# Kernel tuning notes

Measured on AMD Instinct MI355X. Metric: run time of the kernel, lower is better.

Reference implementation:

```python
import jax, jax.numpy as jnp
import numpy as np

N_EMBED = 512
HEAD_SIZE = 64

def setup_inputs() -> dict:
    key = jax.random.key(0)
    k1, k2, k3, k4 = jax.random.split(key, 4)
    B, T, C, H = 4, 4096, N_EMBED, HEAD_SIZE
    x = jax.random.normal(k1, (B, T, C), dtype=jnp.float32)
    # nn.Linear(C, H, bias=False): weight shape [H, C]; y = x @ W.T
    scale = 1.0 / np.sqrt(C)
    Wq = jax.random.uniform(k2, (H, C), dtype=jnp.float32, minval=-scale, maxval=scale)
    Wk = jax.random.uniform(k3, (H, C), dtype=jnp.float32, minval=-scale, maxval=scale)
    Wv = jax.random.uniform(k4, (H, C), dtype=jnp.float32, minval=-scale, maxval=scale)
    return {"x": x, "Wq": Wq, "Wk": Wk, "Wv": Wv}

def reference(x, Wq, Wk, Wv) -> jnp.ndarray:
    B, T, C = x.shape
    q = jnp.einsum('btc,hc->bth', x, Wq)   # [B,T,H]
    k = jnp.einsum('btc,hc->bth', x, Wk)
    v = jnp.einsum('btc,hc->bth', x, Wv)
    # NOTE: original scales by n_embed**-0.5 (C), not head_size**-0.5
    wei = jnp.einsum('bth,bsh->bts', q, k) * (C ** -0.5)  # [B,T,T]
    causal = jnp.tril(jnp.ones((T, T), dtype=bool))
    wei = jnp.where(causal, wei, -jnp.inf)
    wei = jax.nn.softmax(wei, axis=-1)
    out = jnp.einsum('bts,bsh->bth', wei, v)  # [B,T,H]
    return out
```

## Files before the change

kernel.cpp:

```cpp
#include <hip/hip_runtime.h>

typedef float f32x4 __attribute__((ext_vector_type(4)));
typedef __bf16 bf16x8 __attribute__((ext_vector_type(8)));
typedef __bf16 bf16x4 __attribute__((ext_vector_type(4)));
typedef short short4v __attribute__((ext_vector_type(4)));

#define MFMA32K(a, b, c) __builtin_amdgcn_mfma_f32_16x16x32_bf16((a), (b), (c), 0, 0, 0)
#define MFMA16K(a, b, c) __builtin_amdgcn_mfma_f32_16x16x16bf16_1k((a), (b), (c), 0, 0, 0)
#define CFENCE() asm volatile("" ::: "memory")
#define DSFENCE() asm volatile("s_waitcnt lgkmcnt(0)" ::: "memory")

constexpr int Tn = 4096, Cn = 512, Hn = 64;
constexpr float QSCALE = 1.4426950408889634f * 0.04419417382415922f;
constexpr float M0 = -30000.0f;

__global__ void wconv(const float* __restrict__ Wq, const float* __restrict__ Wk,
                      const float* __restrict__ Wv, __bf16* __restrict__ Wb) {
    int t = blockIdx.y;
    int i = blockIdx.x * 256 + threadIdx.x;
    const float* src = (t == 0) ? Wq : (t == 1) ? Wk : Wv;
    float scale = (t == 0) ? QSCALE : 1.0f;
    Wb[t * Hn * Cn + i] = (__bf16)(src[i] * scale);
}

__device__ inline bf16x8 cvt8(float4 u0, float4 u1) {
    bf16x8 r;
    r[0] = (__bf16)u0.x; r[1] = (__bf16)u0.y; r[2] = (__bf16)u0.z; r[3] = (__bf16)u0.w;
    r[4] = (__bf16)u1.x; r[5] = (__bf16)u1.y; r[6] = (__bf16)u1.z; r[7] = (__bf16)u1.w;
    return r;
}

__global__ __launch_bounds__(256) void proj(const float* __restrict__ x,
                                            const __bf16* __restrict__ Wb,
                                            __bf16* __restrict__ Qb,
                                            __bf16* __restrict__ Kb,
                                            __bf16* __restrict__ VF) {
    const int tid = threadIdx.x;
    const int lane = tid & 63, wid = tid >> 6;
    const int c = lane & 15, h = lane >> 4;
    const int row0 = blockIdx.x * 64 + wid * 16;

    __shared__ __bf16 Ws[2][192 * 36];
    __shared__ __bf16 tb[4][16][72];

    f32x4 acc[3][4] = {};
    const float* xr = x + (size_t)(row0 + c) * Cn;

#pragma unroll
    for (int i = 0; i < 3; ++i) {
        int g = tid + i * 256, r = g >> 2, gc = g & 3;
        *(bf16x8*)&Ws[0][r * 36 + gc * 8] = *(const bf16x8*)(Wb + (size_t)r * Cn + gc * 8);
    }
    float4 xc0 = *(const float4*)(xr + 8 * h);
    float4 xc1 = *(const float4*)(xr + 8 * h + 4);
    __syncthreads();

#pragma unroll 2
    for (int ks = 0; ks < 16; ++ks) {
        const int cur = ks & 1;
        bf16x8 wreg[3];
        float4 xn0, xn1;
        if (ks < 15) {
#pragma unroll
            for (int i = 0; i < 3; ++i) {
                int g = tid + i * 256, r = g >> 2, gc = g & 3;
                wreg[i] = *(const bf16x8*)(Wb + (size_t)r * Cn + (ks + 1) * 32 + gc * 8);
            }
            xn0 = *(const float4*)(xr + (ks + 1) * 32 + 8 * h);
            xn1 = *(const float4*)(xr + (ks + 1) * 32 + 8 * h + 4);
        }
        bf16x8 a0 = cvt8(xc0, xc1);
#pragma unroll
        for (int w = 0; w < 3; ++w)
#pragma unroll
            for (int nt = 0; nt < 4; ++nt) {
                bf16x8 bf = *(const bf16x8*)&Ws[cur][(w * 64 + nt * 16 + c) * 36 + 8 * h];
                acc[w][nt] = MFMA32K(a0, bf, acc[w][nt]);
            }
        if (ks < 15) {
#pragma unroll
            for (int i = 0; i < 3; ++i) {
                int g = tid + i * 256, r = g >> 2, gc = g & 3;
                *(bf16x8*)&Ws[cur ^ 1][r * 36 + gc * 8] = wreg[i];
            }
            xc0 = xn0; xc1 = xn1;
        }
        __syncthreads();
    }

#pragma unroll
    for (int w = 0; w < 2; ++w) {
        CFENCE();
#pragma unroll
        for (int nt = 0; nt < 4; ++nt)
#pragma unroll
            for (int r = 0; r < 4; ++r)
                tb[wid][h * 4 + r][nt * 16 + c] = (__bf16)acc[w][nt][r];
        DSFENCE();
        __bf16* dst = (w == 0) ? Qb : Kb;
#pragma unroll
        for (int ch = 0; ch < 2; ++ch) {
            int rr = ch * 8 + (lane >> 3);
            bf16x8 vv = *(const bf16x8*)(&tb[wid][rr][(lane & 7) * 8]);
            *(bf16x8*)(dst + (size_t)(row0 + rr) * Hn + (lane & 7) * 8) = vv;
        }
        CFENCE();
    }

    const int b = row0 >> 12;
    const int t0 = row0 & (Tn - 1);
    const int tile = t0 >> 4;
#pragma unroll
    for (int nt = 0; nt < 4; ++nt) {
        f32x4 a = acc[2][nt];
        bf16x4 v4;
        v4[0] = (__bf16)a.x; v4[1] = (__bf16)a.y;
        v4[2] = (__bf16)a.z; v4[3] = (__bf16)a.w;
        size_t off = ((size_t)((b * 256 + tile) * 4 + h) * 64 + (nt * 16 + c)) * 4;
        *(bf16x4*)(VF + off) = v4;
    }
}

__global__ __launch_bounds__(512) void attn(const __bf16* __restrict__ Qb,
                                            const __bf16* __restrict__ Kb,
                                            const __bf16* __restrict__ VF,
                                            float* __restrict__ out) {
    const int tid = threadIdx.x;
    const int lane = tid & 63, ks = tid >> 6;
    const int c = lane & 15, h = lane >> 4;
    const int b = blockIdx.x & 3;
    const int v = blockIdx.x >> 2;

    const __bf16* Kbase = Kb + (size_t)b * Tn * Hn;
    const __bf16* Vbase = VF + (size_t)b * 256 * 1024;

    __shared__ float Mo[4][64][36];
    __shared__ float Mml[4][64][4];

#pragma unroll 1
    for (int grp = 0; grp < 2; ++grp) {
        const int vg = grp ? (127 - v) : v;
        const int qbase = vg * 32;
        const int nkv = vg / 2 + 1;

        bf16x8 qf[2][2];
#pragma unroll
        for (int qs = 0; qs < 2; ++qs) {
            const __bf16* qp = Qb + (size_t)(b * Tn + qbase + qs * 16 + c) * Hn;
            qf[qs][0] = *(const bf16x8*)(qp + 8 * h);
            qf[qs][1] = *(const bf16x8*)(qp + 32 + 8 * h);
        }

        f32x4 o[2][4] = {};
        float m[2] = {M0, M0};
        float l[2] = {};

        bf16x8 kfc[4][2];
        {
            const int kt0 = (ks < nkv) ? ks : nkv - 1;
#pragma unroll
            for (int ct = 0; ct < 4; ++ct) {
                const __bf16* kp = Kbase + (size_t)(kt0 * 64 + ct * 16 + c) * Hn;
                kfc[ct][0] = *(const bf16x8*)(kp + 8 * h);
                kfc[ct][1] = *(const bf16x8*)(kp + 32 + 8 * h);
            }
        }

        for (int kt = ks; kt < nkv; kt += 8) {
            const int j0 = kt * 64;
            bf16x8 kfn[4][2];
            {
                const int ktn = (kt + 8 < nkv) ? kt + 8 : kt;
#pragma unroll
                for (int ct = 0; ct < 4; ++ct) {
                    const __bf16* kp = Kbase + (size_t)(ktn * 64 + ct * 16 + c) * Hn;
                    kfn[ct][0] = *(const bf16x8*)(kp + 8 * h);
                    kfn[ct][1] = *(const bf16x8*)(kp + 32 + 8 * h);
                }
            }
            short4v vf[4][4];
            const __bf16* vt = Vbase + ((size_t)(j0 >> 4) << 10) + (h << 8);
#pragma unroll
            for (int dt = 0; dt < 4; ++dt)
#pragma unroll
                for (int ct = 0; ct < 4; ++ct)
                    vf[dt][ct] = *(const short4v*)(vt + (ct << 10) + ((dt * 16 + c) << 2));

            const bool diag = (kt == nkv - 1);

#pragma unroll
            for (int qs = 0; qs < 2; ++qs) {
                f32x4 s[4];
#pragma unroll
                for (int ct = 0; ct < 4; ++ct) {
                    f32x4 z = {};
                    z = MFMA32K(kfc[ct][0], qf[qs][0], z);
                    z = MFMA32K(kfc[ct][1], qf[qs][1], z);
                    s[ct] = z;
                }
                if (diag) {
#pragma unroll
                    for (int ct = 0; ct < 4; ++ct)
#pragma unroll
                        for (int r = 0; r < 4; ++r)
                            if (j0 + ct * 16 + 4 * h + r > qbase + qs * 16 + c)
                                s[ct][r] = -1e30f;
                }
                float lm = fmaxf(fmaxf(fmaxf(s[0][0], s[0][1]), fmaxf(s[0][2], s[0][3])),
                                 fmaxf(fmaxf(s[1][0], s[1][1]), fmaxf(s[1][2], s[1][3])));
                lm = fmaxf(lm, fmaxf(fmaxf(fmaxf(s[2][0], s[2][1]), fmaxf(s[2][2], s[2][3])),
                                     fmaxf(fmaxf(s[3][0], s[3][1]), fmaxf(s[3][2], s[3][3]))));
                if (!__all(lm <= m[qs] + 8.0f)) {
                    float rm = fmaxf(lm, __shfl_xor(lm, 16));
                    rm = fmaxf(rm, __shfl_xor(rm, 32));
                    float mn = fmaxf(m[qs], rm);
                    float sc = __builtin_amdgcn_exp2f(m[qs] - mn);
                    m[qs] = mn;
                    l[qs] *= sc;
#pragma unroll
                    for (int dt = 0; dt < 4; ++dt) o[qs][dt] *= sc;
                }
                short4v pf[4];
                float lsum = 0.0f;
#pragma unroll
                for (int ct = 0; ct < 4; ++ct) {
                    bf16x4 pb;
#pragma unroll
                    for (int r = 0; r < 4; ++r) {
                        float p = __builtin_amdgcn_exp2f(s[ct][r] - m[qs]);
                        lsum += p;
                        pb[r] = (__bf16)p;
                    }
                    pf[ct] = __builtin_bit_cast(short4v, pb);
                }
                l[qs] += lsum;
#pragma unroll
                for (int dt = 0; dt < 4; ++dt)
#pragma unroll
                    for (int ct = 0; ct < 4; ++ct)
                        o[qs][dt] = MFMA16K(vf[dt][ct], pf[ct], o[qs][dt]);
            }
#pragma unroll
            for (int ct = 0; ct < 4; ++ct) {
                kfc[ct][0] = kfn[ct][0];
                kfc[ct][1] = kfn[ct][1];
            }
        }

#pragma unroll
        for (int qs = 0; qs < 2; ++qs) {
            l[qs] += __shfl_xor(l[qs], 16);
            l[qs] += __shfl_xor(l[qs], 32);
        }

#pragma unroll
        for (int step = 4; step >= 1; step >>= 1) {
            if (ks >= step && ks < 2 * step) {
                int slot = ks - step;
#pragma unroll
                for (int qs = 0; qs < 2; ++qs) {
                    Mml[slot][lane][qs] = m[qs];
                    Mml[slot][lane][2 + qs] = l[qs];
#pragma unroll
                    for (int dt = 0; dt < 4; ++dt)
                        *(f32x4*)&Mo[slot][lane][(qs * 4 + dt) * 4] = o[qs][dt];
                }
            }
            __syncthreads();
            if (ks < step) {
#pragma unroll
                for (int qs = 0; qs < 2; ++qs) {
                    float m2 = Mml[ks][lane][qs];
                    float l2 = Mml[ks][lane][2 + qs];
                    float M = fmaxf(m[qs], m2);
                    float e1 = __builtin_amdgcn_exp2f(m[qs] - M);
                    float e2 = __builtin_amdgcn_exp2f(m2 - M);
                    m[qs] = M;
                    l[qs] = l[qs] * e1 + l2 * e2;
#pragma unroll
                    for (int dt = 0; dt < 4; ++dt) {
                        f32x4 o2 = *(const f32x4*)&Mo[ks][lane][(qs * 4 + dt) * 4];
                        o[qs][dt] = o[qs][dt] * e1 + o2 * e2;
                    }
                }
            }
            __syncthreads();
        }

        if (ks == 0) {
#pragma unroll
            for (int qs = 0; qs < 2; ++qs) {
                float rl = 1.0f / l[qs];
                float* ob = out + ((size_t)(b * Tn + qbase + qs * 16 + c)) * Hn;
#pragma unroll
                for (int dt = 0; dt < 4; ++dt) {
                    f32x4 w = o[qs][dt] * rl;
                    *(f32x4*)(ob + dt * 16 + 4 * h) = w;
                }
            }
        }
    }
}

extern "C" void kernel_launch(void* const* d_in, const int* in_sizes, int n_in,
                              void* d_out, int out_size, void* d_ws, size_t ws_size,
                              hipStream_t stream) {
    const float* x  = (const float*)d_in[0];
    const float* Wq = (const float*)d_in[1];
    const float* Wk = (const float*)d_in[2];
    const float* Wv = (const float*)d_in[3];
    float* out = (float*)d_out;

    char* ws = (char*)d_ws;
    __bf16* Wb = (__bf16*)ws;
    __bf16* Qb = (__bf16*)(ws + 196608);
    __bf16* Kb = (__bf16*)(ws + 196608 + 2097152);
    __bf16* VF = (__bf16*)(ws + 196608 + 2 * 2097152);

    wconv<<<dim3(128, 3), 256, 0, stream>>>(Wq, Wk, Wv, Wb);
    proj<<<256, 256, 0, stream>>>(x, Wb, Qb, Kb, VF);
    attn<<<256, 512, 0, stream>>>(Qb, Kb, VF, out);
}
```

Baseline: 56.37 us.

## Split proj over K across waves and double attn waves per block

The projection kernel now uses 512 blocks of 512 threads. Each of 4 waves per 16-row group computes a quarter of the C dimension, reading weights straight from global memory instead of staging them in LDS, and the partial sums are reduced through shared memory. The attention kernel doubles to 16 waves per block, each striding over key tiles by 16, drops the K-fragment register prefetch, and extends the merge tree to 16 partitions. The goal is more parallelism and latency hiding on 256 CUs, at the cost of more LDS reduction work and less per-wave prefetching.

```diff
diff --git a/kernel.cpp b/kernel.cpp
--- a/kernel.cpp
+++ b/kernel.cpp
@@ -30,101 +30,93 @@
     return r;
 }
 
-__global__ __launch_bounds__(256) void proj(const float* __restrict__ x,
-                                            const __bf16* __restrict__ Wb,
-                                            __bf16* __restrict__ Qb,
-                                            __bf16* __restrict__ Kb,
-                                            __bf16* __restrict__ VF) {
+__global__ __launch_bounds__(512, 4) void proj(const float* __restrict__ x,
+                                               const __bf16* __restrict__ Wb,
+                                               __bf16* __restrict__ Qb,
+                                               __bf16* __restrict__ Kb,
+                                               __bf16* __restrict__ VF) {
     const int tid = threadIdx.x;
     const int lane = tid & 63, wid = tid >> 6;
+    const int rg = wid >> 2, kc = wid & 3;
     const int c = lane & 15, h = lane >> 4;
-    const int row0 = blockIdx.x * 64 + wid * 16;
-
-    __shared__ __bf16 Ws[2][192 * 36];
-    __shared__ __bf16 tb[4][16][72];
+    const int row0 = blockIdx.x * 32 + rg * 16;
+
+    __shared__ float sl[2][3][64][48];
+    __shared__ __bf16 tb[2][16][72];
 
     f32x4 acc[3][4] = {};
-    const float* xr = x + (size_t)(row0 + c) * Cn;
-
-#pragma unroll
-    for (int i = 0; i < 3; ++i) {
-        int g = tid + i * 256, r = g >> 2, gc = g & 3;
-        *(bf16x8*)&Ws[0][r * 36 + gc * 8] = *(const bf16x8*)(Wb + (size_t)r * Cn + gc * 8);
-    }
-    float4 xc0 = *(const float4*)(xr + 8 * h);
-    float4 xc1 = *(const float4*)(xr + 8 * h + 4);
+    const float* xr = x + (size_t)(row0 + c) * Cn + kc * 128;
+    const __bf16* wr = Wb + kc * 128 + 8 * h;
+
+#pragma unroll
+    for (int it = 0; it < 4; ++it) {
+        const int kb = it * 32 + 8 * h;
+        const float4* p0 = (const float4*)(xr + kb);
+        bf16x8 a0 = cvt8(p0[0], p0[1]);
+#pragma unroll
+        for (int w = 0; w < 3; ++w)
+#pragma unroll
+            for (int nt = 0; nt < 4; ++nt) {
+                bf16x8 bf = *(const bf16x8*)(wr + (size_t)(w * Hn + nt * 16 + c) * Cn + it * 32);
+                acc[w][nt] = MFMA32K(a0, bf, acc[w][nt]);
+            }
+    }
+
+    if (kc) {
+#pragma unroll
+        for (int w = 0; w < 3; ++w)
+#pragma unroll
+            for (int nt = 0; nt < 4; ++nt)
+                *(f32x4*)&sl[rg][kc - 1][lane][(w * 4 + nt) * 4] = acc[w][nt];
+    }
     __syncthreads();
-
-#pragma unroll 2
-    for (int ks = 0; ks < 16; ++ks) {
-        const int cur = ks & 1;
-        bf16x8 wreg[3];
-        float4 xn0, xn1;
-        if (ks < 15) {
-#pragma unroll
-            for (int i = 0; i < 3; ++i) {
-                int g = tid + i * 256, r = g >> 2, gc = g & 3;
-                wreg[i] = *(const bf16x8*)(Wb + (size_t)r * Cn + (ks + 1) * 32 + gc * 8);
-            }
-            xn0 = *(const float4*)(xr + (ks + 1) * 32 + 8 * h);
-            xn1 = *(const float4*)(xr + (ks + 1) * 32 + 8 * h + 4);
-        }
-        bf16x8 a0 = cvt8(xc0, xc1);
-#pragma unroll
-        for (int w = 0; w < 3; ++w)
-#pragma unroll
-            for (int nt = 0; nt < 4; ++nt) {
-                bf16x8 bf = *(const bf16x8*)&Ws[cur][(w * 64 + nt * 16 + c) * 36 + 8 * h];
-                acc[w][nt] = MFMA32K(a0, bf, acc[w][nt]);
-            }
-        if (ks < 15) {
-#pragma unroll
-            for (int i = 0; i < 3; ++i) {
-                int g = tid + i * 256, r = g >> 2, gc = g & 3;
-                *(bf16x8*)&Ws[cur ^ 1][r * 36 + gc * 8] = wreg[i];
-            }
-            xc0 = xn0; xc1 = xn1;
-        }
-        __syncthreads();
-    }
-
-#pragma unroll
-    for (int w = 0; w < 2; ++w) {
-        CFENCE();
-#pragma unroll
-        for (int nt = 0; nt < 4; ++nt)
-#pragma unroll
-            for (int r = 0; r < 4; ++r)
-                tb[wid][h * 4 + r][nt * 16 + c] = (__bf16)acc[w][nt][r];
-        DSFENCE();
-        __bf16* dst = (w == 0) ? Qb : Kb;
-#pragma unroll
-        for (int ch = 0; ch < 2; ++ch) {
-            int rr = ch * 8 + (lane >> 3);
-            bf16x8 vv = *(const bf16x8*)(&tb[wid][rr][(lane & 7) * 8]);
-            *(bf16x8*)(dst + (size_t)(row0 + rr) * Hn + (lane & 7) * 8) = vv;
-        }
-        CFENCE();
-    }
-
-    const int b = row0 >> 12;
-    const int t0 = row0 & (Tn - 1);
-    const int tile = t0 >> 4;
-#pragma unroll
-    for (int nt = 0; nt < 4; ++nt) {
-        f32x4 a = acc[2][nt];
-        bf16x4 v4;
-        v4[0] = (__bf16)a.x; v4[1] = (__bf16)a.y;
-        v4[2] = (__bf16)a.z; v4[3] = (__bf16)a.w;
-        size_t off = ((size_t)((b * 256 + tile) * 4 + h) * 64 + (nt * 16 + c)) * 4;
-        *(bf16x4*)(VF + off) = v4;
-    }
-}
-
-__global__ __launch_bounds__(512) void attn(const __bf16* __restrict__ Qb,
-                                            const __bf16* __restrict__ Kb,
-                                            const __bf16* __restrict__ VF,
-                                            float* __restrict__ out) {
+    if (!kc) {
+#pragma unroll
+        for (int j = 0; j < 3; ++j)
+#pragma unroll
+            for (int w = 0; w < 3; ++w)
+#pragma unroll
+                for (int nt = 0; nt < 4; ++nt)
+                    acc[w][nt] += *(const f32x4*)&sl[rg][j][lane][(w * 4 + nt) * 4];
+
+#pragma unroll
+        for (int w = 0; w < 2; ++w) {
+            CFENCE();
+#pragma unroll
+            for (int nt = 0; nt < 4; ++nt)
+#pragma unroll
+                for (int r = 0; r < 4; ++r)
+                    tb[rg][h * 4 + r][nt * 16 + c] = (__bf16)acc[w][nt][r];
+            DSFENCE();
+            __bf16* dst = (w == 0) ? Qb : Kb;
+#pragma unroll
+            for (int ch = 0; ch < 2; ++ch) {
+                int rr = ch * 8 + (lane >> 3);
+                bf16x8 vv = *(const bf16x8*)(&tb[rg][rr][(lane & 7) * 8]);
+                *(bf16x8*)(dst + (size_t)(row0 + rr) * Hn + (lane & 7) * 8) = vv;
+            }
+            CFENCE();
+        }
+
+        const int b = row0 >> 12;
+        const int t0 = row0 & (Tn - 1);
+        const int tile = t0 >> 4;
+#pragma unroll
+        for (int nt = 0; nt < 4; ++nt) {
+            f32x4 a = acc[2][nt];
+            bf16x4 v4;
+            v4[0] = (__bf16)a.x; v4[1] = (__bf16)a.y;
+            v4[2] = (__bf16)a.z; v4[3] = (__bf16)a.w;
+            size_t off = ((size_t)((b * 256 + tile) * 4 + h) * 64 + (nt * 16 + c)) * 4;
+            *(bf16x4*)(VF + off) = v4;
+        }
+    }
+}
+
+__global__ __launch_bounds__(1024, 4) void attn(const __bf16* __restrict__ Qb,
+                                                const __bf16* __restrict__ Kb,
+                                                const __bf16* __restrict__ VF,
+                                                float* __restrict__ out) {
     const int tid = threadIdx.x;
     const int lane = tid & 63, ks = tid >> 6;
     const int c = lane & 15, h = lane >> 4;
@@ -134,8 +126,8 @@
     const __bf16* Kbase = Kb + (size_t)b * Tn * Hn;
     const __bf16* Vbase = VF + (size_t)b * 256 * 1024;
 
-    __shared__ float Mo[4][64][36];
-    __shared__ float Mml[4][64][4];
+    __shared__ float Mo[8][64][36];
+    __shared__ float Mml[8][64][4];
 
 #pragma unroll 1
     for (int grp = 0; grp < 2; ++grp) {
@@ -155,28 +147,14 @@
         float m[2] = {M0, M0};
         float l[2] = {};
 
-        bf16x8 kfc[4][2];
-        {
-            const int kt0 = (ks < nkv) ? ks : nkv - 1;
+        for (int kt = ks; kt < nkv; kt += 16) {
+            const int j0 = kt * 64;
+            bf16x8 kf[4][2];
 #pragma unroll
             for (int ct = 0; ct < 4; ++ct) {
-                const __bf16* kp = Kbase + (size_t)(kt0 * 64 + ct * 16 + c) * Hn;
-                kfc[ct][0] = *(const bf16x8*)(kp + 8 * h);
-                kfc[ct][1] = *(const bf16x8*)(kp + 32 + 8 * h);
-            }
-        }
-
-        for (int kt = ks; kt < nkv; kt += 8) {
-            const int j0 = kt * 64;
-            bf16x8 kfn[4][2];
-            {
-                const int ktn = (kt + 8 < nkv) ? kt + 8 : kt;
-#pragma unroll
-                for (int ct = 0; ct < 4; ++ct) {
-                    const __bf16* kp = Kbase + (size_t)(ktn * 64 + ct * 16 + c) * Hn;
-                    kfn[ct][0] = *(const bf16x8*)(kp + 8 * h);
-                    kfn[ct][1] = *(const bf16x8*)(kp + 32 + 8 * h);
-                }
+                const __bf16* kp = Kbase + (size_t)(j0 + ct * 16 + c) * Hn;
+                kf[ct][0] = *(const bf16x8*)(kp + 8 * h);
+                kf[ct][1] = *(const bf16x8*)(kp + 32 + 8 * h);
             }
             short4v vf[4][4];
             const __bf16* vt = Vbase + ((size_t)(j0 >> 4) << 10) + (h << 8);
@@ -194,8 +172,8 @@
 #pragma unroll
                 for (int ct = 0; ct < 4; ++ct) {
                     f32x4 z = {};
-                    z = MFMA32K(kfc[ct][0], qf[qs][0], z);
-                    z = MFMA32K(kfc[ct][1], qf[qs][1], z);
+                    z = MFMA32K(kf[ct][0], qf[qs][0], z);
+                    z = MFMA32K(kf[ct][1], qf[qs][1], z);
                     s[ct] = z;
                 }
                 if (diag) {
@@ -240,11 +218,6 @@
                     for (int ct = 0; ct < 4; ++ct)
                         o[qs][dt] = MFMA16K(vf[dt][ct], pf[ct], o[qs][dt]);
             }
-#pragma unroll
-            for (int ct = 0; ct < 4; ++ct) {
-                kfc[ct][0] = kfn[ct][0];
-                kfc[ct][1] = kfn[ct][1];
-            }
         }
 
 #pragma unroll
@@ -254,7 +227,7 @@
         }
 
 #pragma unroll
-        for (int step = 4; step >= 1; step >>= 1) {
+        for (int step = 8; step >= 1; step >>= 1) {
             if (ks >= step && ks < 2 * step) {
                 int slot = ks - step;
 #pragma unroll
@@ -318,6 +291,6 @@
     __bf16* VF = (__bf16*)(ws + 196608 + 2 * 2097152);
 
     wconv<<<dim3(128, 3), 256, 0, stream>>>(Wq, Wk, Wv, Wb);
-    proj<<<256, 256, 0, stream>>>(x, Wb, Qb, Kb, VF);
-    attn<<<256, 512, 0, stream>>>(Qb, Kb, VF, out);
-}
+    proj<<<512, 512, 0, stream>>>(x, Wb, Qb, Kb, VF);
+    attn<<<256, 1024, 0, stream>>>(Qb, Kb, VF, out);
+}
```

After: 136.2 us. 2.42x slower.

## Stage x tile through swizzled LDS with coalesced loads in projection kernel

Applied to the files above, without the earlier changes.

The projection kernel now loads a 64-row x tile cooperatively with coalesced float4 reads, converts it to bf16 and stores it in LDS with an XOR swizzle alongside the weight tile. The K step grows from 32 to 64 per iteration, which halves the iterations and barriers. Previously each lane read x rows directly from global memory with strided per-row accesses. This trades more LDS traffic and a larger shared footprint (64KB) for better global coalescing and bank-conflict-free fragment reads.

```diff
diff --git a/kernel.cpp b/kernel.cpp
--- a/kernel.cpp
+++ b/kernel.cpp
@@ -23,13 +23,6 @@
     Wb[t * Hn * Cn + i] = (__bf16)(src[i] * scale);
 }
 
-__device__ inline bf16x8 cvt8(float4 u0, float4 u1) {
-    bf16x8 r;
-    r[0] = (__bf16)u0.x; r[1] = (__bf16)u0.y; r[2] = (__bf16)u0.z; r[3] = (__bf16)u0.w;
-    r[4] = (__bf16)u1.x; r[5] = (__bf16)u1.y; r[6] = (__bf16)u1.z; r[7] = (__bf16)u1.w;
-    return r;
-}
-
 __global__ __launch_bounds__(256) void proj(const float* __restrict__ x,
                                             const __bf16* __restrict__ Wb,
                                             __bf16* __restrict__ Qb,
@@ -38,56 +31,77 @@
     const int tid = threadIdx.x;
     const int lane = tid & 63, wid = tid >> 6;
     const int c = lane & 15, h = lane >> 4;
-    const int row0 = blockIdx.x * 64 + wid * 16;
-
-    __shared__ __bf16 Ws[2][192 * 36];
-    __shared__ __bf16 tb[4][16][72];
-
-    f32x4 acc[3][4] = {};
-    const float* xr = x + (size_t)(row0 + c) * Cn;
-
-#pragma unroll
-    for (int i = 0; i < 3; ++i) {
-        int g = tid + i * 256, r = g >> 2, gc = g & 3;
-        *(bf16x8*)&Ws[0][r * 36 + gc * 8] = *(const bf16x8*)(Wb + (size_t)r * Cn + gc * 8);
-    }
-    float4 xc0 = *(const float4*)(xr + 8 * h);
-    float4 xc1 = *(const float4*)(xr + 8 * h + 4);
+    const int row0 = blockIdx.x * 64;
+
+    __shared__ __bf16 lds[2][16384];
+
+    f32x4 acc[12] = {};
+    float4 xl[4];
+    bf16x8 wl[6];
+
+    auto load_x = [&](int ks) {
+#pragma unroll
+        for (int p = 0; p < 4; ++p) {
+            int g = tid + p * 256;
+            int row = g >> 4, cidx = g & 15;
+            xl[p] = *(const float4*)(x + (size_t)(row0 + row) * Cn + ks * 64 + cidx * 4);
+        }
+    };
+    auto load_w = [&](int ks) {
+#pragma unroll
+        for (int s = 0; s < 6; ++s) {
+            int L = tid + s * 256;
+            int ch = L >> 3, q = L & 7;
+            wl[s] = *(const bf16x8*)(Wb + (size_t)ch * Cn + ks * 64 + q * 8);
+        }
+    };
+    auto store_buf = [&](int buf) {
+        char* base = (char*)lds[buf];
+#pragma unroll
+        for (int p = 0; p < 4; ++p) {
+            int g = tid + p * 256;
+            int row = g >> 4, cidx = g & 15;
+            bf16x4 b;
+            b[0] = (__bf16)xl[p].x; b[1] = (__bf16)xl[p].y;
+            b[2] = (__bf16)xl[p].z; b[3] = (__bf16)xl[p].w;
+            *(bf16x4*)(base + row * 128 +
+                       ((((cidx >> 1) ^ (row & 7)) << 4) | ((cidx & 1) << 3))) = b;
+        }
+        char* bb = base + 8192;
+#pragma unroll
+        for (int s = 0; s < 6; ++s) {
+            int L = tid + s * 256;
+            int ch = L >> 3, q = L & 7;
+            *(bf16x8*)(bb + ch * 128 + ((q ^ (ch & 7)) << 4)) = wl[s];
+        }
+    };
+
+    load_x(0); load_w(0);
+    store_buf(0);
     __syncthreads();
 
-#pragma unroll 2
-    for (int ks = 0; ks < 16; ++ks) {
+    for (int ks = 0; ks < 8; ++ks) {
         const int cur = ks & 1;
-        bf16x8 wreg[3];
-        float4 xn0, xn1;
-        if (ks < 15) {
-#pragma unroll
-            for (int i = 0; i < 3; ++i) {
-                int g = tid + i * 256, r = g >> 2, gc = g & 3;
-                wreg[i] = *(const bf16x8*)(Wb + (size_t)r * Cn + (ks + 1) * 32 + gc * 8);
-            }
-            xn0 = *(const float4*)(xr + (ks + 1) * 32 + 8 * h);
-            xn1 = *(const float4*)(xr + (ks + 1) * 32 + 8 * h + 4);
-        }
-        bf16x8 a0 = cvt8(xc0, xc1);
-#pragma unroll
-        for (int w = 0; w < 3; ++w)
-#pragma unroll
-            for (int nt = 0; nt < 4; ++nt) {
-                bf16x8 bf = *(const bf16x8*)&Ws[cur][(w * 64 + nt * 16 + c) * 36 + 8 * h];
-                acc[w][nt] = MFMA32K(a0, bf, acc[w][nt]);
-            }
-        if (ks < 15) {
-#pragma unroll
-            for (int i = 0; i < 3; ++i) {
-                int g = tid + i * 256, r = g >> 2, gc = g & 3;
-                *(bf16x8*)&Ws[cur ^ 1][r * 36 + gc * 8] = wreg[i];
-            }
-            xc0 = xn0; xc1 = xn1;
-        }
+        if (ks < 7) { load_x(ks + 1); load_w(ks + 1); }
+        const char* A = (const char*)lds[cur];
+        const char* B = A + 8192;
+#pragma unroll
+        for (int k = 0; k < 2; ++k) {
+            bf16x8 af = *(const bf16x8*)(A + (wid * 16 + c) * 128 +
+                                         (((4 * k + h) ^ (c & 7)) << 4));
+#pragma unroll
+            for (int j = 0; j < 12; ++j) {
+                int ch = j * 16 + c;
+                bf16x8 bf = *(const bf16x8*)(B + ch * 128 +
+                                             (((4 * k + h) ^ (ch & 7)) << 4));
+                acc[j] = MFMA32K(af, bf, acc[j]);
+            }
+        }
+        if (ks < 7) store_buf(cur ^ 1);
         __syncthreads();
     }
 
+    __bf16(*tb)[16][72] = (__bf16(*)[16][72])lds[0];
 #pragma unroll
     for (int w = 0; w < 2; ++w) {
         CFENCE();
@@ -95,24 +109,24 @@
         for (int nt = 0; nt < 4; ++nt)
 #pragma unroll
             for (int r = 0; r < 4; ++r)
-                tb[wid][h * 4 + r][nt * 16 + c] = (__bf16)acc[w][nt][r];
+                tb[wid][h * 4 + r][nt * 16 + c] = (__bf16)acc[w * 4 + nt][r];
         DSFENCE();
         __bf16* dst = (w == 0) ? Qb : Kb;
 #pragma unroll
-        for (int ch = 0; ch < 2; ++ch) {
-            int rr = ch * 8 + (lane >> 3);
+        for (int ch2 = 0; ch2 < 2; ++ch2) {
+            int rr = ch2 * 8 + (lane >> 3);
             bf16x8 vv = *(const bf16x8*)(&tb[wid][rr][(lane & 7) * 8]);
-            *(bf16x8*)(dst + (size_t)(row0 + rr) * Hn + (lane & 7) * 8) = vv;
+            *(bf16x8*)(dst + (size_t)(row0 + wid * 16 + rr) * Hn + (lane & 7) * 8) = vv;
         }
         CFENCE();
     }
-
-    const int b = row0 >> 12;
-    const int t0 = row0 & (Tn - 1);
+    const int rowv = row0 + wid * 16;
+    const int b = rowv >> 12;
+    const int t0 = rowv & (Tn - 1);
     const int tile = t0 >> 4;
 #pragma unroll
     for (int nt = 0; nt < 4; ++nt) {
-        f32x4 a = acc[2][nt];
+        f32x4 a = acc[8 + nt];
         bf16x4 v4;
         v4[0] = (__bf16)a.x; v4[1] = (__bf16)a.y;
         v4[2] = (__bf16)a.z; v4[3] = (__bf16)a.w;
```

Result: no change. 56.29 us (-0.1%).
